# Performance work log

Measured on AMD Instinct MI355X. Metric: run time of the kernel, lower is better.

## Reference

```python
import jax, jax.numpy as jnp
import numpy as np

N_QUBITS = 12
N_LAYERS = 6
BATCH = 8192
D_IN = 512


def _apply_1q(state, gate, wire):
    # state: [B] + [2]*n (real), gate: [2,2]. new[j] = sum_i gate[j,i]*old[i]
    s = jnp.moveaxis(state, 1 + wire, -1)
    s = jnp.einsum('...i,ji->...j', s, gate)
    return jnp.moveaxis(s, -1, 1 + wire)


def _apply_cnot(state, ctrl, tgt):
    # flip target amplitude pair where control bit == 1
    s = jnp.moveaxis(state, (1 + ctrl, 1 + tgt), (-2, -1))
    s = jnp.concatenate([s[..., :1, :], s[..., 1:, ::-1]], axis=-2)
    return jnp.moveaxis(s, (-2, -1), (1 + ctrl, 1 + tgt))


def _simulate(angles, weights):
    # angles: [B, n] per-sample RY angles; weights: [L, n] shared RY angles.
    # Circuit: H + RY(angle) per wire on |0>, then L x (RY layer + CNOT chain).
    # All gates are real -> real float32 statevector.
    B, n = angles.shape
    L = weights.shape[0]
    inv_sqrt2 = jnp.float32(1.0 / np.sqrt(2.0))
    half = 0.5 * angles
    c, s = jnp.cos(half), jnp.sin(half)
    # per-wire single-qubit state RY(a) @ H @ |0> = inv_sqrt2 * [c-s, c+s]
    v = inv_sqrt2 * jnp.stack([c - s, c + s], axis=-1)  # [B, n, 2]
    state = v[:, 0]  # [B, 2]
    for w in range(1, n):
        state = jnp.einsum('b...,bj->b...j', state, v[:, w])  # product state
    # state: [B] + [2]*n
    for layer in range(L):
        h = 0.5 * weights[layer]
        cl, sl = jnp.cos(h), jnp.sin(h)
        for w in range(n):
            gate = jnp.stack([jnp.stack([cl[w], -sl[w]]),
                              jnp.stack([sl[w], cl[w]])])
            state = _apply_1q(state, gate, w)
        for w in range(n - 1):
            state = _apply_cnot(state, w, w + 1)
    probs = state * state
    zs = []
    for w in range(n):
        axes = tuple(a for a in range(1, n + 1) if a != 1 + w)
        p = probs.sum(axis=axes)  # [B, 2]
        zs.append(p[:, 0] - p[:, 1])
    return jnp.stack(zs, axis=-1)  # [B, n] = <Z_i>


def setup_inputs() -> dict:
    key = jax.random.key(0)
    ks = jax.random.split(key, 6)
    x = jax.random.normal(ks[0], (BATCH, D_IN), jnp.float32)
    pre_w = jax.random.normal(ks[1], (N_QUBITS, D_IN), jnp.float32) / np.sqrt(D_IN)
    pre_b = jax.random.normal(ks[2], (N_QUBITS,), jnp.float32) * 0.01
    weights = jax.random.normal(ks[3], (N_LAYERS, N_QUBITS), jnp.float32)
    post_w = jax.random.normal(ks[4], (1, N_QUBITS), jnp.float32) / np.sqrt(N_QUBITS)
    post_b = jax.random.normal(ks[5], (1,), jnp.float32) * 0.01
    return {"x": x, "pre_w": pre_w, "pre_b": pre_b, "weights": weights,
            "post_w": post_w, "post_b": post_b}


def reference(x, pre_w, pre_b, weights, post_w, post_b):
    pre = x @ pre_w.T + pre_b                # [B, n_qubits]
    angles = pre * jnp.float32(np.pi / 2.0)  # RY(inputs[i]*pi/2)
    q_out = _simulate(angles, weights)       # [B, n_qubits]
    return q_out @ post_w.T + post_b         # [B, 1]
```

## Files before the change

### kernel.cpp

```cpp
#include <hip/hip_runtime.h>
#include <math.h>

#define NQ 12
#define NL 6
#define BATCHN 8192
#define DIN 512

typedef _Float16 f16;
typedef __attribute__((ext_vector_type(8)))  _Float16 f16x8;
typedef __attribute__((ext_vector_type(16))) float    f32x16;
typedef unsigned int u32;
typedef __attribute__((ext_vector_type(4))) u32 u32x4;
typedef __attribute__((ext_vector_type(2))) int i32x2;


__device__ __forceinline__ u32 pkrtz(float a, float b) {
  auto p = __builtin_amdgcn_cvt_pkrtz(a, b);
  return __builtin_bit_cast(u32, p);
}
__device__ __forceinline__ u32 bperm(int addr, u32 v) {
  return (u32)__builtin_amdgcn_ds_bpermute(addr, (int)v);
}
__device__ __forceinline__ float dppx1(float v) {
  return __int_as_float(__builtin_amdgcn_mov_dpp(__float_as_int(v), 0xB1, 0xF, 0xF, true));
}
__device__ __forceinline__ u32 dppx1u(u32 v) {
  return (u32)__builtin_amdgcn_mov_dpp((int)v, 0xB1, 0xF, 0xF, true);
}
__device__ __forceinline__ float dppx2(float v) {
  return __int_as_float(__builtin_amdgcn_mov_dpp(__float_as_int(v), 0x4E, 0xF, 0xF, true));
}
__device__ __forceinline__ float dppx8(float v) {
  return __int_as_float(__builtin_amdgcn_mov_dpp(__float_as_int(v), 0x128, 0xF, 0xF, true));
}
template <int PAT>
__device__ __forceinline__ float swzf(float v) {
  return __int_as_float(__builtin_amdgcn_ds_swizzle(__float_as_int(v), PAT));
}

#if __has_builtin(__builtin_amdgcn_permlane32_swap)
__device__ __forceinline__ void pswap(u32& a, u32& b) {
  i32x2 r = __builtin_amdgcn_permlane32_swap((int)a, (int)b, false, false);
  a = (u32)r.x; b = (u32)r.y;
}
#else
#define PSWAP_FALLBACK 1
__device__ __forceinline__ void pswap_fb(u32& a, u32& b, bool hi, int axor) {
  u32 xa = bperm(axor, a), xb = bperm(axor, b);
  u32 na = hi ? xb : a;
  u32 nb = hi ? b : xa;
  a = na; b = nb;
}
#endif

__device__ __forceinline__ float wave_sum(float v) {
  v += dppx1(v);
  v += dppx2(v);
  v += swzf<0x101F>(v);
  v += dppx8(v);
  v += swzf<0x401F>(v);
#ifndef PSWAP_FALLBACK
  u32 a = __builtin_bit_cast(u32, v), b = a;
  pswap(a, b);
  return __builtin_bit_cast(float, a) + __builtin_bit_cast(float, b);
#else
  return v + __shfl_xor(v, 32, 64);
#endif
}
__device__ __forceinline__ f16x8 asf(const u32 a[4]) {
  u32x4 v; v.x = a[0]; v.y = a[1]; v.z = a[2]; v.w = a[3];
  return __builtin_bit_cast(f16x8, v);
}
__device__ __forceinline__ f16x8 ldB(const u32* __restrict__ p, int off) {
  u32x4 v = *(const u32x4*)(p + off);
  return __builtin_bit_cast(f16x8, v);
}

#if __has_builtin(__builtin_amdgcn_global_load_lds)
#define HAVE_GLLDS 1
__device__ __forceinline__ void stage_mat(const u32* __restrict__ Bg,
                                          u32* lbuf, int wid, int lane) {
  #pragma unroll
  for (int c2 = 0; c2 < 2; ++c2) {
    const int c = wid * 2 + c2;
    const u32* g = Bg + c * 256 + lane * 4;
    u32* l = lbuf + c * 256;
    __builtin_amdgcn_global_load_lds(
        (const __attribute__((address_space(1))) u32*)g,
        (__attribute__((address_space(3))) u32*)l, 16, 0, 0);
  }
}
#else
__device__ __forceinline__ void stage_mat(const u32* __restrict__ Bg,
                                          u32* lbuf, int wid, int lane) {
  #pragma unroll
  for (int c2 = 0; c2 < 2; ++c2) {
    const int c = wid * 2 + c2;
    u32x4 v = *(const u32x4*)(Bg + c * 256 + lane * 4);
    *(u32x4*)(lbuf + c * 256 + lane * 4) = v;
  }
}
#endif

__device__ __forceinline__ void sincos_rev(float rev, float* s, float* c) {
  float r = rev - floorf(rev);
#if __has_builtin(__builtin_amdgcn_sinf) && __has_builtin(__builtin_amdgcn_cosf)
  *s = __builtin_amdgcn_sinf(r);
  *c = __builtin_amdgcn_cosf(r);
#else
  const float TWO_PI = 6.28318530717958647693f;
  sincosf(r * TWO_PI, s, c);
#endif
}

__device__ __forceinline__ u32 foldw(u32 w, u32 m) {
  u32 partner = dppx1u(w);
  return (m & partner) | (~m & w);
}

__global__ void setup_mats(const float* __restrict__ weights, u32* __restrict__ Bbuf) {
  const int mm = blockIdx.x >> 3;
  const int l  = mm >> 1;
  const int qs = mm & 1;
  __shared__ float c6[6], s6[6];
  if (threadIdx.x < 6) {
    float h = 0.5f * weights[l * NQ + qs * 6 + threadIdx.x];
    c6[threadIdx.x] = cosf(h);
    s6[threadIdx.x] = sinf(h);
  }
  __syncthreads();
  const int t = (blockIdx.x & 7) * 256 + threadIdx.x;
  const int lane = (t >> 2) & 63;
  const int fk   = t >> 8;
  const int kt   = fk & 3;
  const int nt   = fk >> 2;
  const int n     = nt * 32 + (lane & 31);
  const int kbase = kt * 16 + (lane >> 5) * 8 + (t & 3) * 2;
  float v[2];
  #pragma unroll
  for (int u = 0; u < 2; ++u) {
    int k = kbase + u;
    int bb = k;
    if (l >= 1) { bb ^= bb << 1; bb ^= bb << 2; bb ^= bb << 4; bb &= 63; }
    float prod = 1.f;
    #pragma unroll
    for (int w = 0; w < 6; ++w) {
      const int aw = (n >> w) & 1, bw = (bb >> w) & 1;
      prod *= (aw == bw) ? c6[w] : (aw ? s6[w] : -s6[w]);
    }
    v[u] = prod;
  }
  Bbuf[mm * 2048 + t] = pkrtz(v[0], v[1]);
}

template <bool FOLD>
__device__ __forceinline__ void mm_step(f32x16 (&d)[2][2],
                                        const u32* Bl,
                                        u32 maskA, u32 maskB) {
  f16x8 Bc0 = ldB(Bl, 0 * 256);
  f16x8 Bc1 = ldB(Bl, 4 * 256);
  u32 fr[2][4][4];
  #pragma unroll
  for (int kt = 0; kt < 4; ++kt) {
    const int s  = kt >> 1;
    const int b0 = 4 * ((2 * kt) & 3);
    const int b1 = 4 * ((2 * kt + 1) & 3);
    #pragma unroll
    for (int mt = 0; mt < 2; ++mt) {
      u32 p0a = pkrtz(d[s][mt][b0 + 0], d[s][mt][b0 + 1]);
      u32 p0b = pkrtz(d[s][mt][b0 + 2], d[s][mt][b0 + 3]);
      u32 p1a = pkrtz(d[s][mt][b1 + 0], d[s][mt][b1 + 1]);
      u32 p1b = pkrtz(d[s][mt][b1 + 2], d[s][mt][b1 + 3]);
      if (FOLD) {
        const int PAR4[4] = {0, 1, 1, 0};
        const int ka = (PAR4[b0 >> 2] + s) & 1;
        const int kc = (PAR4[b1 >> 2] + s) & 1;
        p0a = foldw(p0a, ka ? maskB : maskA);
        p0b = foldw(p0b, ka ? maskA : maskB);
        p1a = foldw(p1a, kc ? maskB : maskA);
        p1b = foldw(p1b, kc ? maskA : maskB);
      }
#ifdef PSWAP_FALLBACK
      pswap_fb(p0a, p1a, false, 0);
      pswap_fb(p0b, p1b, false, 0);
#else
      pswap(p0a, p1a);
      pswap(p0b, p1b);
#endif
      fr[mt][kt][0] = p0a;
      fr[mt][kt][1] = p0b;
      fr[mt][kt][2] = p1a;
      fr[mt][kt][3] = p1b;
    }
  }
  #pragma unroll
  for (int kt = 0; kt < 4; ++kt) {
    f16x8 B0 = Bc0, B1 = Bc1;
    if (kt < 3) {
      Bc0 = ldB(Bl, (kt + 1) * 256);
      Bc1 = ldB(Bl, (4 + kt + 1) * 256);
    }
    f16x8 A0 = asf(fr[0][kt]);
    f16x8 A1 = asf(fr[1][kt]);
    if (kt == 0) {
      f32x16 z{};
      d[0][0] = __builtin_amdgcn_mfma_f32_32x32x16_f16(A0, B0, z, 0, 0, 0);
      d[0][1] = __builtin_amdgcn_mfma_f32_32x32x16_f16(A0, B1, z, 0, 0, 0);
      d[1][0] = __builtin_amdgcn_mfma_f32_32x32x16_f16(A1, B0, z, 0, 0, 0);
      d[1][1] = __builtin_amdgcn_mfma_f32_32x32x16_f16(A1, B1, z, 0, 0, 0);
    } else {
      d[0][0] = __builtin_amdgcn_mfma_f32_32x32x16_f16(A0, B0, d[0][0], 0, 0, 0);
      d[0][1] = __builtin_amdgcn_mfma_f32_32x32x16_f16(A0, B1, d[0][1], 0, 0, 0);
      d[1][0] = __builtin_amdgcn_mfma_f32_32x32x16_f16(A1, B0, d[1][0], 0, 0, 0);
      d[1][1] = __builtin_amdgcn_mfma_f32_32x32x16_f16(A1, B1, d[1][1], 0, 0, 0);
    }
  }
}

__global__ void __launch_bounds__(256) __attribute__((amdgpu_waves_per_eu(4, 8)))
dqc_main(const float* __restrict__ x,
         const float* __restrict__ pre_w,
         const float* __restrict__ pre_b,
         const float* __restrict__ weights,
         const float* __restrict__ post_w,
         const float* __restrict__ post_b,
         const u32* __restrict__ Bbuf,
         float* __restrict__ out)
{
  const int lane = threadIdx.x & 63;
  const int wid  = threadIdx.x >> 6;
  const bool hi  = lane >= 32;
  const int b    = blockIdx.x * 4 + wid;
  const u32 maskA = hi ? 0x0000FFFFu : 0xFFFF0000u;
  const u32 maskB = ~maskA;

  __shared__ __align__(16) u32 Bs[2][2048];
  stage_mat(Bbuf + 2 * 2048, &Bs[0][0], wid, lane);
  stage_mat(Bbuf + 3 * 2048, &Bs[1][0], wid, lane);

  float acc[NQ];
  const float* xr = x + (size_t)b * DIN + lane * 8;
  const float4 xa = *(const float4*)(xr);
  const float4 xb = *(const float4*)(xr + 4);
  #pragma unroll
  for (int w = 0; w < NQ; ++w) {
    const float* wr = pre_w + w * DIN + lane * 8;
    const float4 wa = *(const float4*)(wr);
    const float4 wb = *(const float4*)(wr + 4);
    acc[w] = xa.x * wa.x + xa.y * wa.y + xa.z * wa.z + xa.w * wa.w
           + xb.x * wb.x + xb.y * wb.y + xb.z * wb.z + xb.w * wb.w;
  }
  #pragma unroll
  for (int w = 0; w < NQ; ++w) acc[w] = wave_sum(acc[w]);

  const float INV_4PI = 0.07957747154594766788f;
  float u0[NQ], u1[NQ];
  #pragma unroll
  for (int w = 0; w < NQ; ++w) {
    const float cw2 = 0.125f + pre_b[w] * 0.125f + weights[w] * INV_4PI;
    const float rev = fmaf(acc[w], 0.125f, cw2);
    sincos_rev(rev, &u1[w], &u0[w]);
  }

  float base8[8];
  #pragma unroll
  for (int j = 0; j < 8; ++j)
    base8[j] = ((j & 1) ? u1[0] : u0[0]) * ((j & 2) ? u1[1] : u0[1]) * ((j & 4) ? u1[2] : u0[2]);
  float hiP[4];
  #pragma unroll
  for (int kt = 0; kt < 4; ++kt)
    hiP[kt] = (hi ? u1[3] : u0[3]) * ((kt & 1) ? u1[4] : u0[4]) * ((kt & 2) ? u1[5] : u0[5]);
  const float q5 = ((lane & 2) ? u1[7] : u0[7]) * ((lane & 4) ? u1[8] : u0[8])
                 * ((lane & 8) ? u1[9] : u0[9]) * ((lane & 16) ? u1[10] : u0[10]);
  const float qA = q5 * ((lane & 1) ? u1[6] : u0[6]);
  const float qB = q5 * ((lane & 1) ? u0[6] : u1[6]);
  const float qeven = hi ? qB : qA;
  const float qodd  = hi ? qA : qB;
  const float qe0 = qeven * u0[11], qo0 = qodd * u0[11];
  const float qe1 = qeven * u1[11], qo1 = qodd * u1[11];

  asm volatile("s_waitcnt vmcnt(0)" ::: "memory");
  __syncthreads();

  const u32* B0p = &Bs[0][0] + lane * 4;
  const u32* B1p = &Bs[1][0] + lane * 4;

  f32x16 d[2][2];
  {
    f16x8 Ic0 = ldB(B0p, 0 * 256);
    f16x8 Ic1 = ldB(B0p, 4 * 256);
    const int PKT[4] = {0, 1, 1, 0};
    const int PDW[4] = {0, 1, 1, 0};
    #pragma unroll
    for (int kt = 0; kt < 4; ++kt) {
      u32 a0[4], a1[4];
      #pragma unroll
      for (int dw = 0; dw < 4; ++dw) {
        const float e0 = base8[2 * dw] * hiP[kt];
        const float e1 = base8[2 * dw + 1] * hiP[kt];
        const bool cls = (PKT[kt] ^ PDW[dw]) != 0;
        a0[dw] = pkrtz((cls ? qo0 : qe0) * e0, (cls ? qe0 : qo0) * e1);
        a1[dw] = pkrtz((cls ? qo1 : qe1) * e0, (cls ? qe1 : qo1) * e1);
      }
      f16x8 B0 = Ic0, B1 = Ic1;
      if (kt < 3) {
        Ic0 = ldB(B0p, (kt + 1) * 256);
        Ic1 = ldB(B0p, (4 + kt + 1) * 256);
      }
      f16x8 A0 = asf(a0), A1 = asf(a1);
      if (kt == 0) {
        f32x16 z{};
        d[0][0] = __builtin_amdgcn_mfma_f32_32x32x16_f16(A0, B0, z, 0, 0, 0);
        d[0][1] = __builtin_amdgcn_mfma_f32_32x32x16_f16(A0, B1, z, 0, 0, 0);
        d[1][0] = __builtin_amdgcn_mfma_f32_32x32x16_f16(A1, B0, z, 0, 0, 0);
        d[1][1] = __builtin_amdgcn_mfma_f32_32x32x16_f16(A1, B1, z, 0, 0, 0);
      } else {
        d[0][0] = __builtin_amdgcn_mfma_f32_32x32x16_f16(A0, B0, d[0][0], 0, 0, 0);
        d[0][1] = __builtin_amdgcn_mfma_f32_32x32x16_f16(A0, B1, d[0][1], 0, 0, 0);
        d[1][0] = __builtin_amdgcn_mfma_f32_32x32x16_f16(A1, B0, d[1][0], 0, 0, 0);
        d[1][1] = __builtin_amdgcn_mfma_f32_32x32x16_f16(A1, B1, d[1][1], 0, 0, 0);
      }
    }
  }

  #define STEP_TAIL(nextmm, bufidx)                                  \
    do {                                                             \
      asm volatile("s_waitcnt vmcnt(0)" ::: "memory");               \
      __syncthreads();                                               \
      stage_mat(Bbuf + (nextmm) * 2048, &Bs[bufidx][0], wid, lane);  \
    } while (0)

  STEP_TAIL(4, 0);
  mm_step<false>(d, B1p, maskA, maskB);
  STEP_TAIL(5, 1);
  mm_step<true >(d, B0p, maskA, maskB);
  STEP_TAIL(6, 0);
  mm_step<false>(d, B1p, maskA, maskB);
  STEP_TAIL(7, 1);
  mm_step<true >(d, B0p, maskA, maskB);
  STEP_TAIL(8, 0);
  mm_step<false>(d, B1p, maskA, maskB);
  STEP_TAIL(9, 1);
  mm_step<true >(d, B0p, maskA, maskB);
  STEP_TAIL(10, 0);
  mm_step<false>(d, B1p, maskA, maskB);
  STEP_TAIL(11, 1);
  mm_step<true >(d, B0p, maskA, maskB);
  asm volatile("s_waitcnt vmcnt(0)" ::: "memory");
  __syncthreads();
  mm_step<false>(d, B1p, maskA, maskB);
  #undef STEP_TAIL

  const float pw0 = post_w[0], pw1 = post_w[1], pw2 = post_w[2],
              pw3 = post_w[3], pw4 = post_w[4], pw5 = post_w[5];
  float A0s = 0.f, A1s = 0.f, s00 = 0.f, s01 = 0.f, accA = 0.f, accB = 0.f;
  #pragma unroll
  for (int mt = 0; mt < 2; ++mt)
    #pragma unroll
    for (int nt = 0; nt < 2; ++nt)
      #pragma unroll
      for (int r = 0; r < 16; ++r) {
        float v = d[mt][nt][r];
        float sq = v * v;
        const int par0 = (__builtin_popcount(r & 3) + __builtin_popcount(r >> 2) + mt) & 1;
        if (par0) A1s += sq; else A0s += sq;
        if (nt == 0) { if (par0) s01 += sq; else s00 += sq; }
        const int c0 = r & 1;
        const int c1 = (r ^ (r >> 1)) & 1;
        const int c3 = c1 ^ ((r >> 2) & 1);
        const int c4 = c3 ^ ((r >> 3) & 1);
        const int c5 = c4 ^ mt;
        const float ca = (c0 ? -pw0 : pw0) + (c1 ? -pw1 : pw1);
        const float cb = (c1 ? -pw2 : pw2) + (c3 ? -pw3 : pw3)
                       + (c4 ? -pw4 : pw4) + (c5 ? -pw5 : pw5);
        accA = fmaf(ca, sq, accA);
        accB = fmaf(cb, sq, accB);
      }
  const float sgnhi = hi ? -1.f : 1.f;
  const float tot   = A0s + A1s;
  const float diff  = sgnhi * (A0s - A1s);
  const float diffs = sgnhi * (2.f * (s00 - s01) - (A0s - A1s));
  float Sq = 0.f;
  #pragma unroll
  for (int j = 0; j < 5; ++j) {
    const int par = __builtin_popcount(lane & ((2 << j) - 1)) & 1;
    Sq += par ? -post_w[6 + j] : post_w[6 + j];
  }
  const float s5 = (__builtin_popcount(lane & 31) & 1) ? -post_w[11] : post_w[11];
  const float zcomb = accA + sgnhi * accB + diff * Sq + diffs * s5;

  const float tots = wave_sum(tot);
  const float zs   = wave_sum(zcomb);

  if (lane == 0) {
    out[b] = fmaf(zs, 1.0f / tots, post_b[0]);
  }
}

extern "C" void kernel_launch(void* const* d_in, const int* in_sizes, int n_in,
                              void* d_out, int out_size, void* d_ws, size_t ws_size,
                              hipStream_t stream) {
  (void)in_sizes; (void)n_in; (void)out_size; (void)ws_size;
  const float* x       = (const float*)d_in[0];
  const float* pre_w   = (const float*)d_in[1];
  const float* pre_b   = (const float*)d_in[2];
  const float* weights = (const float*)d_in[3];
  const float* post_w  = (const float*)d_in[4];
  const float* post_b  = (const float*)d_in[5];
  float* out = (float*)d_out;
  u32* Bbuf = (u32*)d_ws;

  setup_mats<<<96, 256, 0, stream>>>(weights, Bbuf);
  dqc_main<<<BATCHN / 4, 256, 0, stream>>>(x, pre_w, pre_b, weights,
                                           post_w, post_b, Bbuf, out);
}
```

Before: 115.0 us.

## Process two batch samples per wave to amortize LDS matrix staging and syncs

```diff
diff --git a/kernel.cpp b/kernel.cpp
--- a/kernel.cpp
+++ b/kernel.cpp
@@ -18,9 +18,6 @@
   auto p = __builtin_amdgcn_cvt_pkrtz(a, b);
   return __builtin_bit_cast(u32, p);
 }
-__device__ __forceinline__ u32 bperm(int addr, u32 v) {
-  return (u32)__builtin_amdgcn_ds_bpermute(addr, (int)v);
-}
 __device__ __forceinline__ float dppx1(float v) {
   return __int_as_float(__builtin_amdgcn_mov_dpp(__float_as_int(v), 0xB1, 0xF, 0xF, true));
 }
@@ -46,7 +43,8 @@
 #else
 #define PSWAP_FALLBACK 1
 __device__ __forceinline__ void pswap_fb(u32& a, u32& b, bool hi, int axor) {
-  u32 xa = bperm(axor, a), xb = bperm(axor, b);
+  u32 xa = (u32)__builtin_amdgcn_ds_bpermute(axor, (int)a);
+  u32 xb = (u32)__builtin_amdgcn_ds_bpermute(axor, (int)b);
   u32 na = hi ? xb : a;
   u32 nb = hi ? b : xa;
   a = na; b = nb;
@@ -71,13 +69,12 @@
   u32x4 v; v.x = a[0]; v.y = a[1]; v.z = a[2]; v.w = a[3];
   return __builtin_bit_cast(f16x8, v);
 }
-__device__ __forceinline__ f16x8 ldB(const u32* __restrict__ p, int off) {
+__device__ __forceinline__ f16x8 ldB(const u32* p, int off) {
   u32x4 v = *(const u32x4*)(p + off);
   return __builtin_bit_cast(f16x8, v);
 }
 
 #if __has_builtin(__builtin_amdgcn_global_load_lds)
-#define HAVE_GLLDS 1
 __device__ __forceinline__ void stage_mat(const u32* __restrict__ Bg,
                                           u32* lbuf, int wid, int lane) {
   #pragma unroll
@@ -154,9 +151,9 @@
 }
 
 template <bool FOLD>
-__device__ __forceinline__ void mm_step(f32x16 (&d)[2][2],
-                                        const u32* Bl,
-                                        u32 maskA, u32 maskB) {
+__device__ __forceinline__ void mm_one(f32x16 (&d)[2][2],
+                                       const u32* Bl,
+                                       u32 maskA, u32 maskB) {
   f16x8 Bc0 = ldB(Bl, 0 * 256);
   f16x8 Bc1 = ldB(Bl, 4 * 256);
   u32 fr[2][4][4];
@@ -217,42 +214,11 @@
   }
 }
 
-__global__ void __launch_bounds__(256) __attribute__((amdgpu_waves_per_eu(4, 8)))
-dqc_main(const float* __restrict__ x,
-         const float* __restrict__ pre_w,
-         const float* __restrict__ pre_b,
-         const float* __restrict__ weights,
-         const float* __restrict__ post_w,
-         const float* __restrict__ post_b,
-         const u32* __restrict__ Bbuf,
-         float* __restrict__ out)
-{
-  const int lane = threadIdx.x & 63;
-  const int wid  = threadIdx.x >> 6;
-  const bool hi  = lane >= 32;
-  const int b    = blockIdx.x * 4 + wid;
-  const u32 maskA = hi ? 0x0000FFFFu : 0xFFFF0000u;
-  const u32 maskB = ~maskA;
-
-  __shared__ __align__(16) u32 Bs[2][2048];
-  stage_mat(Bbuf + 2 * 2048, &Bs[0][0], wid, lane);
-  stage_mat(Bbuf + 3 * 2048, &Bs[1][0], wid, lane);
-
-  float acc[NQ];
-  const float* xr = x + (size_t)b * DIN + lane * 8;
-  const float4 xa = *(const float4*)(xr);
-  const float4 xb = *(const float4*)(xr + 4);
-  #pragma unroll
-  for (int w = 0; w < NQ; ++w) {
-    const float* wr = pre_w + w * DIN + lane * 8;
-    const float4 wa = *(const float4*)(wr);
-    const float4 wb = *(const float4*)(wr + 4);
-    acc[w] = xa.x * wa.x + xa.y * wa.y + xa.z * wa.z + xa.w * wa.w
-           + xb.x * wb.x + xb.y * wb.y + xb.z * wb.z + xb.w * wb.w;
-  }
-  #pragma unroll
-  for (int w = 0; w < NQ; ++w) acc[w] = wave_sum(acc[w]);
-
+__device__ __forceinline__ void build_scal(const float (&acc)[NQ],
+    const float* __restrict__ pre_b, const float* __restrict__ weights,
+    int lane, bool hi,
+    float (&base8)[8], float (&hiP)[4],
+    float& qe0, float& qo0, float& qe1, float& qo1) {
   const float INV_4PI = 0.07957747154594766788f;
   float u0[NQ], u1[NQ];
   #pragma unroll
@@ -261,12 +227,9 @@
     const float rev = fmaf(acc[w], 0.125f, cw2);
     sincos_rev(rev, &u1[w], &u0[w]);
   }
-
-  float base8[8];
   #pragma unroll
   for (int j = 0; j < 8; ++j)
     base8[j] = ((j & 1) ? u1[0] : u0[0]) * ((j & 2) ? u1[1] : u0[1]) * ((j & 4) ? u1[2] : u0[2]);
-  float hiP[4];
   #pragma unroll
   for (int kt = 0; kt < 4; ++kt)
     hiP[kt] = (hi ? u1[3] : u0[3]) * ((kt & 1) ? u1[4] : u0[4]) * ((kt & 2) ? u1[5] : u0[5]);
@@ -276,81 +239,53 @@
   const float qB = q5 * ((lane & 1) ? u0[6] : u1[6]);
   const float qeven = hi ? qB : qA;
   const float qodd  = hi ? qA : qB;
-  const float qe0 = qeven * u0[11], qo0 = qodd * u0[11];
-  const float qe1 = qeven * u1[11], qo1 = qodd * u1[11];
-
-  asm volatile("s_waitcnt vmcnt(0)" ::: "memory");
-  __syncthreads();
-
-  const u32* B0p = &Bs[0][0] + lane * 4;
-  const u32* B1p = &Bs[1][0] + lane * 4;
-
-  f32x16 d[2][2];
-  {
-    f16x8 Ic0 = ldB(B0p, 0 * 256);
-    f16x8 Ic1 = ldB(B0p, 4 * 256);
-    const int PKT[4] = {0, 1, 1, 0};
-    const int PDW[4] = {0, 1, 1, 0};
+  qe0 = qeven * u0[11]; qo0 = qodd * u0[11];
+  qe1 = qeven * u1[11]; qo1 = qodd * u1[11];
+}
+
+__device__ __forceinline__ void init_mm2(f32x16 (&d)[2][2], const u32* Bp0,
+    const float (&base8)[8], const float (&hiP)[4],
+    float qe0, float qo0, float qe1, float qo1) {
+  f16x8 Ic0 = ldB(Bp0, 0 * 256);
+  f16x8 Ic1 = ldB(Bp0, 4 * 256);
+  const int PKT[4] = {0, 1, 1, 0};
+  const int PDW[4] = {0, 1, 1, 0};
+  #pragma unroll
+  for (int kt = 0; kt < 4; ++kt) {
+    u32 a0[4], a1[4];
     #pragma unroll
-    for (int kt = 0; kt < 4; ++kt) {
-      u32 a0[4], a1[4];
-      #pragma unroll
-      for (int dw = 0; dw < 4; ++dw) {
-        const float e0 = base8[2 * dw] * hiP[kt];
-        const float e1 = base8[2 * dw + 1] * hiP[kt];
-        const bool cls = (PKT[kt] ^ PDW[dw]) != 0;
-        a0[dw] = pkrtz((cls ? qo0 : qe0) * e0, (cls ? qe0 : qo0) * e1);
-        a1[dw] = pkrtz((cls ? qo1 : qe1) * e0, (cls ? qe1 : qo1) * e1);
-      }
-      f16x8 B0 = Ic0, B1 = Ic1;
-      if (kt < 3) {
-        Ic0 = ldB(B0p, (kt + 1) * 256);
-        Ic1 = ldB(B0p, (4 + kt + 1) * 256);
-      }
-      f16x8 A0 = asf(a0), A1 = asf(a1);
-      if (kt == 0) {
-        f32x16 z{};
-        d[0][0] = __builtin_amdgcn_mfma_f32_32x32x16_f16(A0, B0, z, 0, 0, 0);
-        d[0][1] = __builtin_amdgcn_mfma_f32_32x32x16_f16(A0, B1, z, 0, 0, 0);
-        d[1][0] = __builtin_amdgcn_mfma_f32_32x32x16_f16(A1, B0, z, 0, 0, 0);
-        d[1][1] = __builtin_amdgcn_mfma_f32_32x32x16_f16(A1, B1, z, 0, 0, 0);
-      } else {
-        d[0][0] = __builtin_amdgcn_mfma_f32_32x32x16_f16(A0, B0, d[0][0], 0, 0, 0);
-        d[0][1] = __builtin_amdgcn_mfma_f32_32x32x16_f16(A0, B1, d[0][1], 0, 0, 0);
-        d[1][0] = __builtin_amdgcn_mfma_f32_32x32x16_f16(A1, B0, d[1][0], 0, 0, 0);
-        d[1][1] = __builtin_amdgcn_mfma_f32_32x32x16_f16(A1, B1, d[1][1], 0, 0, 0);
-      }
-    }
-  }
-
-  #define STEP_TAIL(nextmm, bufidx)                                  \
-    do {                                                             \
-      asm volatile("s_waitcnt vmcnt(0)" ::: "memory");               \
-      __syncthreads();                                               \
-      stage_mat(Bbuf + (nextmm) * 2048, &Bs[bufidx][0], wid, lane);  \
-    } while (0)
-
-  STEP_TAIL(4, 0);
-  mm_step<false>(d, B1p, maskA, maskB);
-  STEP_TAIL(5, 1);
-  mm_step<true >(d, B0p, maskA, maskB);
-  STEP_TAIL(6, 0);
-  mm_step<false>(d, B1p, maskA, maskB);
-  STEP_TAIL(7, 1);
-  mm_step<true >(d, B0p, maskA, maskB);
-  STEP_TAIL(8, 0);
-  mm_step<false>(d, B1p, maskA, maskB);
-  STEP_TAIL(9, 1);
-  mm_step<true >(d, B0p, maskA, maskB);
-  STEP_TAIL(10, 0);
-  mm_step<false>(d, B1p, maskA, maskB);
-  STEP_TAIL(11, 1);
-  mm_step<true >(d, B0p, maskA, maskB);
-  asm volatile("s_waitcnt vmcnt(0)" ::: "memory");
-  __syncthreads();
-  mm_step<false>(d, B1p, maskA, maskB);
-  #undef STEP_TAIL
-
+    for (int dw = 0; dw < 4; ++dw) {
+      const float e0 = base8[2 * dw] * hiP[kt];
+      const float e1 = base8[2 * dw + 1] * hiP[kt];
+      const bool cls = (PKT[kt] ^ PDW[dw]) != 0;
+      a0[dw] = pkrtz((cls ? qo0 : qe0) * e0, (cls ? qe0 : qo0) * e1);
+      a1[dw] = pkrtz((cls ? qo1 : qe1) * e0, (cls ? qe1 : qo1) * e1);
+    }
+    f16x8 B0 = Ic0, B1 = Ic1;
+    if (kt < 3) {
+      Ic0 = ldB(Bp0, (kt + 1) * 256);
+      Ic1 = ldB(Bp0, (4 + kt + 1) * 256);
+    }
+    f16x8 A0 = asf(a0), A1 = asf(a1);
+    if (kt == 0) {
+      f32x16 z{};
+      d[0][0] = __builtin_amdgcn_mfma_f32_32x32x16_f16(A0, B0, z, 0, 0, 0);
+      d[0][1] = __builtin_amdgcn_mfma_f32_32x32x16_f16(A0, B1, z, 0, 0, 0);
+      d[1][0] = __builtin_amdgcn_mfma_f32_32x32x16_f16(A1, B0, z, 0, 0, 0);
+      d[1][1] = __builtin_amdgcn_mfma_f32_32x32x16_f16(A1, B1, z, 0, 0, 0);
+    } else {
+      d[0][0] = __builtin_amdgcn_mfma_f32_32x32x16_f16(A0, B0, d[0][0], 0, 0, 0);
+      d[0][1] = __builtin_amdgcn_mfma_f32_32x32x16_f16(A0, B1, d[0][1], 0, 0, 0);
+      d[1][0] = __builtin_amdgcn_mfma_f32_32x32x16_f16(A1, B0, d[1][0], 0, 0, 0);
+      d[1][1] = __builtin_amdgcn_mfma_f32_32x32x16_f16(A1, B1, d[1][1], 0, 0, 0);
+    }
+  }
+}
+
+__device__ __forceinline__ void measure(const f32x16 (&d)[2][2], int b,
+    int lane, bool hi,
+    const float* __restrict__ post_w, const float* __restrict__ post_b,
+    float* __restrict__ out) {
   const float pw0 = post_w[0], pw1 = post_w[1], pw2 = post_w[2],
               pw3 = post_w[3], pw4 = post_w[4], pw5 = post_w[5];
   float A0s = 0.f, A1s = 0.f, s00 = 0.f, s01 = 0.f, accA = 0.f, accB = 0.f;
@@ -397,6 +332,106 @@
   }
 }
 
+__global__ void __launch_bounds__(256) __attribute__((amdgpu_waves_per_eu(2, 4)))
+dqc_main(const float* __restrict__ x,
+         const float* __restrict__ pre_w,
+         const float* __restrict__ pre_b,
+         const float* __restrict__ weights,
+         const float* __restrict__ post_w,
+         const float* __restrict__ post_b,
+         const u32* __restrict__ Bbuf,
+         float* __restrict__ out)
+{
+  const int lane = threadIdx.x & 63;
+  const int wid  = threadIdx.x >> 6;
+  const bool hi  = lane >= 32;
+  const int b0   = blockIdx.x * 8 + wid * 2;
+  const int b1   = b0 + 1;
+  const u32 maskA = hi ? 0x0000FFFFu : 0xFFFF0000u;
+  const u32 maskB = ~maskA;
+
+  __shared__ __align__(16) u32 Bs[2][2048];
+  stage_mat(Bbuf + 2 * 2048, &Bs[0][0], wid, lane);
+  stage_mat(Bbuf + 3 * 2048, &Bs[1][0], wid, lane);
+
+  float acc0[NQ], acc1[NQ];
+  const float* xr0 = x + (size_t)b0 * DIN + lane * 8;
+  const float* xr1 = x + (size_t)b1 * DIN + lane * 8;
+  const float4 xa0 = *(const float4*)(xr0);
+  const float4 xb0 = *(const float4*)(xr0 + 4);
+  const float4 xa1 = *(const float4*)(xr1);
+  const float4 xb1 = *(const float4*)(xr1 + 4);
+  #pragma unroll
+  for (int w = 0; w < NQ; ++w) {
+    const float* wr = pre_w + w * DIN + lane * 8;
+    const float4 wa = *(const float4*)(wr);
+    const float4 wb = *(const float4*)(wr + 4);
+    acc0[w] = xa0.x * wa.x + xa0.y * wa.y + xa0.z * wa.z + xa0.w * wa.w
+            + xb0.x * wb.x + xb0.y * wb.y + xb0.z * wb.z + xb0.w * wb.w;
+    acc1[w] = xa1.x * wa.x + xa1.y * wa.y + xa1.z * wa.z + xa1.w * wa.w
+            + xb1.x * wb.x + xb1.y * wb.y + xb1.z * wb.z + xb1.w * wb.w;
+  }
+  #pragma unroll
+  for (int w = 0; w < NQ; ++w) acc0[w] = wave_sum(acc0[w]);
+  #pragma unroll
+  for (int w = 0; w < NQ; ++w) acc1[w] = wave_sum(acc1[w]);
+
+  float b8A[8], hPA[4], qe0A, qo0A, qe1A, qo1A;
+  build_scal(acc0, pre_b, weights, lane, hi, b8A, hPA, qe0A, qo0A, qe1A, qo1A);
+  float b8B[8], hPB[4], qe0B, qo0B, qe1B, qo1B;
+  build_scal(acc1, pre_b, weights, lane, hi, b8B, hPB, qe0B, qo0B, qe1B, qo1B);
+
+  asm volatile("s_waitcnt vmcnt(0)" ::: "memory");
+  __syncthreads();
+
+  const u32* B0p = &Bs[0][0] + lane * 4;
+  const u32* B1p = &Bs[1][0] + lane * 4;
+
+  f32x16 d0[2][2], d1[2][2];
+  init_mm2(d0, B0p, b8A, hPA, qe0A, qo0A, qe1A, qo1A);
+  init_mm2(d1, B0p, b8B, hPB, qe0B, qo0B, qe1B, qo1B);
+
+  #define STEP_TAIL(nextmm, bufidx)                                  \
+    do {                                                             \
+      asm volatile("s_waitcnt vmcnt(0)" ::: "memory");               \
+      __syncthreads();                                               \
+      stage_mat(Bbuf + (nextmm) * 2048, &Bs[bufidx][0], wid, lane);  \
+    } while (0)
+
+  STEP_TAIL(4, 0);
+  mm_one<false>(d0, B1p, maskA, maskB);
+  mm_one<false>(d1, B1p, maskA, maskB);
+  STEP_TAIL(5, 1);
+  mm_one<true >(d0, B0p, maskA, maskB);
+  mm_one<true >(d1, B0p, maskA, maskB);
+  STEP_TAIL(6, 0);
+  mm_one<false>(d0, B1p, maskA, maskB);
+  mm_one<false>(d1, B1p, maskA, maskB);
+  STEP_TAIL(7, 1);
+  mm_one<true >(d0, B0p, maskA, maskB);
+  mm_one<true >(d1, B0p, maskA, maskB);
+  STEP_TAIL(8, 0);
+  mm_one<false>(d0, B1p, maskA, maskB);
+  mm_one<false>(d1, B1p, maskA, maskB);
+  STEP_TAIL(9, 1);
+  mm_one<true >(d0, B0p, maskA, maskB);
+  mm_one<true >(d1, B0p, maskA, maskB);
+  STEP_TAIL(10, 0);
+  mm_one<false>(d0, B1p, maskA, maskB);
+  mm_one<false>(d1, B1p, maskA, maskB);
+  STEP_TAIL(11, 1);
+  mm_one<true >(d0, B0p, maskA, maskB);
+  mm_one<true >(d1, B0p, maskA, maskB);
+  asm volatile("s_waitcnt vmcnt(0)" ::: "memory");
+  __syncthreads();
+  mm_one<false>(d0, B1p, maskA, maskB);
+  mm_one<false>(d1, B1p, maskA, maskB);
+  #undef STEP_TAIL
+
+  measure(d0, b0, lane, hi, post_w, post_b, out);
+  measure(d1, b1, lane, hi, post_w, post_b, out);
+}
+
 extern "C" void kernel_launch(void* const* d_in, const int* in_sizes, int n_in,
                               void* d_out, int out_size, void* d_ws, size_t ws_size,
                               hipStream_t stream) {
@@ -411,6 +446,6 @@
   u32* Bbuf = (u32*)d_ws;
 
   setup_mats<<<96, 256, 0, stream>>>(weights, Bbuf);
-  dqc_main<<<BATCHN / 4, 256, 0, stream>>>(x, pre_w, pre_b, weights,
+  dqc_main<<<BATCHN / 8, 256, 0, stream>>>(x, pre_w, pre_b, weights,
                                            post_w, post_b, Bbuf, out);
 }
```

Result: faster. 112.6 us (-2.1%).
